# Kernel optimization log

Hardware: AMD Instinct MI355X
Metric: run time of the kernel (lower is better)

The kernel has to match this reference:

```python
import jax, jax.numpy as jnp
import numpy as np

F, B, H, N = 2048, 2, 1024, 16
E = H // N  # per-head depth = 64


def setup_inputs() -> dict:
    key = jax.random.key(0)
    k1, k2, k3, k4 = jax.random.split(key, 4)
    q_input = jax.random.normal(k1, (F, B, H), dtype=jnp.float32)
    mask = jax.random.randint(k2, (B, 1, F, F), 0, 2).astype(bool)
    w_qkv = jax.random.normal(k3, (H, 3 * H), dtype=jnp.float32) * 0.02
    b_qkv = jnp.zeros((3 * H,), dtype=jnp.float32)
    w_out = jax.random.normal(k4, (N, E, H), dtype=jnp.float32) * 0.02
    b_out = jnp.zeros((H,), dtype=jnp.float32)
    return {"q_input": q_input, "mask": mask, "w_qkv": w_qkv, "b_qkv": b_qkv,
            "w_out": w_out, "b_out": b_out}


def reference(q_input, mask, w_qkv, b_qkv, w_out, b_out):
    # fused QKV projection: FBH,HD->FBD (+ bias on D)
    qkv = jnp.einsum('fbh,hd->fbd', q_input, w_qkv) + b_qkv          # [F,B,3H]
    qkv = qkv.reshape(F, B, N, 3 * E)
    q, k, v = jnp.split(qkv, 3, axis=-1)                             # each [F,B,N,E]
    scale = 1.0 / jnp.sqrt(jnp.asarray(E, dtype=q.dtype))
    logits = jnp.einsum('fbne,tbne->bnft', q, k) * scale             # [B,N,F,T]
    logits = jnp.where(mask, logits, jnp.asarray(-10000.0, logits.dtype))
    attn_w = jax.nn.softmax(logits, axis=-1)
    ctx = jnp.einsum('bnft,tbne->bnfe', attn_w, v)                   # [B,N,F,E]
    ctx = jnp.transpose(ctx, (2, 0, 1, 3))                           # [F,B,N,E]
    out = jnp.einsum('fbne,ned->fbd', ctx, w_out)                    # [F,B,H] (no bias added)
    return out, b_out
```

## Files before the change

### kernel.cpp

```cpp
#include <hip/hip_runtime.h>
#include <hip/hip_bf16.h>
#include <math.h>

#define F_DIM 2048
#define B_DIM 2
#define H_DIM 1024
#define N_HEADS 16
#define E_DIM 64
#define D3 3072
#define M_DIM 4096

typedef __hip_bfloat16 bf16;
typedef __attribute__((ext_vector_type(8))) __bf16 bf16x8;
typedef __attribute__((ext_vector_type(8))) unsigned short u16x8;
typedef __attribute__((ext_vector_type(4))) float f32x4;

static __device__ __forceinline__ unsigned short f2bf(float f) {
    unsigned u = __float_as_uint(f);
    return (unsigned short)((u + 0x7FFFu + ((u >> 16) & 1u)) >> 16);
}

static __device__ __forceinline__ void glds16(const unsigned short* g, unsigned short* l) {
    __builtin_amdgcn_global_load_lds((const __attribute__((address_space(1))) unsigned int*)g,
                                     (__attribute__((address_space(3))) unsigned int*)l,
                                     16, 0, 0);
}

__global__ void detect_mask_kernel(const int* __restrict__ mask_words, int* __restrict__ flag) {
    __shared__ int red[256];
    int v = mask_words[threadIdx.x];
    red[threadIdx.x] = v & ~1;
    __syncthreads();
    for (int s = 128; s > 0; s >>= 1) {
        if (threadIdx.x < s) red[threadIdx.x] |= red[threadIdx.x + s];
        __syncthreads();
    }
    if (threadIdx.x == 0) *flag = (red[0] != 0) ? 1 : 0;
}

__global__ void pack_mask_kernel(const int* __restrict__ mi, const unsigned char* __restrict__ mu,
                                 const int* __restrict__ flag, unsigned* __restrict__ bits) {
    int w = blockIdx.x * 256 + threadIdx.x;
    size_t base = (size_t)w * 32;
    unsigned out = 0;
    if (*flag) {
        #pragma unroll
        for (int j = 0; j < 32; ++j) out |= (mu[base + j] ? 1u : 0u) << j;
    } else {
        #pragma unroll
        for (int j = 0; j < 32; ++j) out |= (mi[base + j] ? 1u : 0u) << j;
    }
    bits[w] = out;
}

__global__ __launch_bounds__(256) void convert_kernel(const float* __restrict__ in,
                                                      unsigned short* __restrict__ out) {
    int i = (blockIdx.x * 256 + threadIdx.x) * 8;
    float4 a = *(const float4*)&in[i];
    float4 b = *(const float4*)&in[i + 4];
    u16x8 o;
    o[0] = f2bf(a.x); o[1] = f2bf(a.y); o[2] = f2bf(a.z); o[3] = f2bf(a.w);
    o[4] = f2bf(b.x); o[5] = f2bf(b.y); o[6] = f2bf(b.z); o[7] = f2bf(b.w);
    *(u16x8*)&out[i] = o;
}

__global__ __launch_bounds__(256) void transpose_bf16_kernel(const float* __restrict__ in,
                                                             unsigned short* __restrict__ out,
                                                             int R, int C) {
    __shared__ float t[32][33];
    const int c0 = blockIdx.x * 32, r0 = blockIdx.y * 32;
    const int lc = threadIdx.x & 31, lr = threadIdx.x >> 5;
    #pragma unroll
    for (int i = 0; i < 4; ++i) {
        int r = lr + i * 8;
        t[r][lc] = in[(size_t)(r0 + r) * C + c0 + lc];
    }
    __syncthreads();
    #pragma unroll
    for (int i = 0; i < 4; ++i) {
        int r = lr + i * 8;
        out[(size_t)(c0 + r) * R + r0 + lc] = f2bf(t[lc][r]);
    }
}

template<int BM, int BN, bool ADD_BIAS, bool OUT_BF16>
__global__ __launch_bounds__(256) void gemm_bt_kernel(const unsigned short* __restrict__ A,
                                                      const unsigned short* __restrict__ Bt,
                                                      const float* __restrict__ bias,
                                                      void* __restrict__ Cout, int Nc) {
    __shared__ unsigned short Ald[BM * 32];
    __shared__ unsigned short Bld[BN * 32];
    constexpr int WM = BM / 2, WN = BN / 2;
    constexpr int MI = WM / 16, NI = WN / 16;
    constexpr int ACH = BM * 4;
    constexpr int TCH = (BM + BN) * 4;
    const int tid = threadIdx.x;
    const int wave = tid >> 6;
    const int lane = tid & 63;
    const int quad = lane >> 4;
    const int l16 = lane & 15;
    const int wm = (wave & 1) * WM;
    const int wn = (wave >> 1) * WN;
    const int m0 = blockIdx.y * BM;
    const int n0 = blockIdx.x * BN;

    f32x4 acc[MI][NI];
    #pragma unroll
    for (int i = 0; i < MI; ++i)
        #pragma unroll
        for (int j = 0; j < NI; ++j) acc[i][j] = (f32x4){0.f, 0.f, 0.f, 0.f};

    for (int k0 = 0; k0 < 1024; k0 += 32) {
        __syncthreads();
        #pragma unroll
        for (int rr = 0; rr < TCH / 256; ++rr) {
            const int chunk = rr * 256 + tid;
            const int wbase = (rr * 256 + wave * 64) * 8;
            if (chunk < ACH) {
                const int row = chunk >> 2, ko = (chunk & 3) * 8;
                glds16(&A[(size_t)(m0 + row) * 1024 + k0 + ko], &Ald[wbase]);
            } else {
                const int c2 = chunk - ACH;
                const int row = c2 >> 2, ko = (c2 & 3) * 8;
                glds16(&Bt[(size_t)(n0 + row) * 1024 + k0 + ko], &Bld[wbase - ACH * 8]);
            }
        }
        __syncthreads();

        bf16x8 af[MI], bfr[NI];
        #pragma unroll
        for (int i = 0; i < MI; ++i)
            af[i] = *(const bf16x8*)&Ald[(wm + i * 16 + l16) * 32 + quad * 8];
        #pragma unroll
        for (int j = 0; j < NI; ++j)
            bfr[j] = *(const bf16x8*)&Bld[(wn + j * 16 + l16) * 32 + quad * 8];
        #pragma unroll
        for (int mi = 0; mi < MI; ++mi)
            #pragma unroll
            for (int ni = 0; ni < NI; ++ni)
                acc[mi][ni] = __builtin_amdgcn_mfma_f32_16x16x32_bf16(af[mi], bfr[ni], acc[mi][ni], 0, 0, 0);
    }

    #pragma unroll
    for (int ni = 0; ni < NI; ++ni) {
        const int col = n0 + wn + ni * 16 + l16;
        const float bv = ADD_BIAS ? bias[col] : 0.f;
        #pragma unroll
        for (int mi = 0; mi < MI; ++mi) {
            const int rowb = m0 + wm + mi * 16 + quad * 4;
            #pragma unroll
            for (int r = 0; r < 4; ++r) {
                float v = acc[mi][ni][r] + bv;
                if (OUT_BF16) ((unsigned short*)Cout)[(size_t)(rowb + r) * Nc + col] = f2bf(v);
                else          ((float*)Cout)[(size_t)(rowb + r) * Nc + col] = v;
            }
        }
    }
}

#define TT 64
#define LSTR 72
__global__ __launch_bounds__(256) void attn_mfma_kernel(const bf16* __restrict__ qkv_,
                                                        const unsigned* __restrict__ mbits,
                                                        unsigned short* __restrict__ ctxb) {
    __shared__ unsigned short K_lds[TT * LSTR];
    __shared__ unsigned short Vt_lds[E_DIM * LSTR];
    __shared__ unsigned short P_lds[4 * 16 * LSTR];

    const unsigned short* qkv = (const unsigned short*)qkv_;
    const int tid = threadIdx.x;
    const int wave = tid >> 6;
    const int lane = tid & 63;
    const int quad = lane >> 4;
    const int l16 = lane & 15;
    const int f0 = blockIdx.x * 64;
    const int b = blockIdx.y >> 4;
    const int n = blockIdx.y & 15;
    const int head = n * 192;

    bf16x8 qf[2];
    #pragma unroll
    for (int ks = 0; ks < 2; ++ks) {
        int f = f0 + wave * 16 + l16;
        qf[ks] = *(const bf16x8*)&qkv[(size_t)(f * B_DIM + b) * D3 + head + ks * 32 + quad * 8];
    }

    f32x4 O[4];
    #pragma unroll
    for (int ec = 0; ec < 4; ++ec) O[ec] = (f32x4){0.f, 0.f, 0.f, 0.f};
    float lsum[4] = {0.f, 0.f, 0.f, 0.f};

    unsigned short* Pw = P_lds + wave * 16 * LSTR;
    const float c_exp = 0.18033688011112042f;

    for (int t0 = 0; t0 < F_DIM; t0 += TT) {
        __syncthreads();

        #pragma unroll
        for (int i = 0; i < 2; ++i) {
            int c = tid + i * 256;
            int tr = c >> 3, e0 = (c & 7) * 8;
            u16x8 kv = *(const u16x8*)&qkv[(size_t)((t0 + tr) * B_DIM + b) * D3 + head + 64 + e0];
            *(u16x8*)&K_lds[tr * LSTR + e0] = kv;
        }
        {
            int tp = tid & 31, e0 = (tid >> 5) * 8;
            u16x8 v0 = *(const u16x8*)&qkv[(size_t)((t0 + 2 * tp) * B_DIM + b) * D3 + head + 128 + e0];
            u16x8 v1 = *(const u16x8*)&qkv[(size_t)((t0 + 2 * tp + 1) * B_DIM + b) * D3 + head + 128 + e0];
            #pragma unroll
            for (int j = 0; j < 8; ++j) {
                unsigned pk = (unsigned)v0[j] | ((unsigned)v1[j] << 16);
                *(unsigned*)&Vt_lds[(e0 + j) * LSTR + 2 * tp] = pk;
            }
        }
        __syncthreads();

        f32x4 S[4];
        #pragma unroll
        for (int ck = 0; ck < 4; ++ck) S[ck] = (f32x4){0.f, 0.f, 0.f, 0.f};
        #pragma unroll
        for (int ck = 0; ck < 4; ++ck)
            #pragma unroll
            for (int ks = 0; ks < 2; ++ks) {
                bf16x8 kb = *(const bf16x8*)&K_lds[(ck * 16 + l16) * LSTR + ks * 32 + quad * 8];
                S[ck] = __builtin_amdgcn_mfma_f32_16x16x32_bf16(qf[ks], kb, S[ck], 0, 0, 0);
            }

        #pragma unroll
        for (int r = 0; r < 4; ++r) {
            const int row = quad * 4 + r;
            const int f = f0 + wave * 16 + row;
            uint2 wb = *(const uint2*)&mbits[((size_t)b * F_DIM + f) * 64 + (t0 >> 5)];
            #pragma unroll
            for (int ck = 0; ck < 4; ++ck) {
                unsigned wsel = (ck & 2) ? wb.y : wb.x;
                int bit = ((ck & 1) << 4) + l16;
                float p = __builtin_amdgcn_exp2f(S[ck][r] * c_exp);
                p = ((wsel >> bit) & 1u) ? p : 0.f;
                lsum[r] += p;
                Pw[row * LSTR + ck * 16 + l16] = f2bf(p);
            }
        }

        #pragma unroll
        for (int ks = 0; ks < 2; ++ks) {
            bf16x8 pf = *(const bf16x8*)&Pw[l16 * LSTR + ks * 32 + quad * 8];
            #pragma unroll
            for (int ec = 0; ec < 4; ++ec) {
                bf16x8 vb = *(const bf16x8*)&Vt_lds[(ec * 16 + l16) * LSTR + ks * 32 + quad * 8];
                O[ec] = __builtin_amdgcn_mfma_f32_16x16x32_bf16(pf, vb, O[ec], 0, 0, 0);
            }
        }
    }

    #pragma unroll
    for (int r = 0; r < 4; ++r) {
        float l = lsum[r];
        #pragma unroll
        for (int d = 1; d < 16; d <<= 1) l += __shfl_xor(l, d);
        const int f = f0 + wave * 16 + quad * 4 + r;
        const float inv = 1.0f / l;
        #pragma unroll
        for (int ec = 0; ec < 4; ++ec) {
            ctxb[(size_t)(f * B_DIM + b) * H_DIM + n * 64 + ec * 16 + l16] = f2bf(O[ec][r] * inv);
        }
    }
}

__global__ void bout_copy_kernel(const float* __restrict__ b_out, float* __restrict__ dst) {
    int h = blockIdx.x * 256 + threadIdx.x;
    if (h < H_DIM) dst[h] = b_out[h];
}

extern "C" void kernel_launch(void* const* d_in, const int* in_sizes, int n_in,
                              void* d_out, int out_size, void* d_ws, size_t ws_size,
                              hipStream_t stream) {
    const float* q_input = (const float*)d_in[0];
    const void*  mask    = d_in[1];
    const float* w_qkv   = (const float*)d_in[2];
    const float* b_qkv   = (const float*)d_in[3];
    const float* w_out   = (const float*)d_in[4];
    const float* b_out   = (const float*)d_in[5];
    float* out = (float*)d_out;

    char* ws = (char*)d_ws;
    bf16*           qkv     = (bf16*)ws;
    unsigned short* qin_bf  = (unsigned short*)(ws + 25165824);
    unsigned short* ctx     = qin_bf;
    unsigned short* wqkv_bt = (unsigned short*)(ws + 33554432);
    unsigned short* wout_bt = wqkv_bt;
    unsigned*       mbits   = (unsigned*)(ws + 39845888);
    int*            flag    = (int*)(ws + 40894464);

    detect_mask_kernel<<<1, 256, 0, stream>>>((const int*)mask, flag);
    pack_mask_kernel<<<1024, 256, 0, stream>>>((const int*)mask, (const unsigned char*)mask, flag, mbits);

    convert_kernel<<<2048, 256, 0, stream>>>(q_input, qin_bf);
    transpose_bf16_kernel<<<dim3(96, 32), 256, 0, stream>>>(w_qkv, wqkv_bt, 1024, 3072);

    gemm_bt_kernel<128, 128, true, true><<<dim3(24, 32), 256, 0, stream>>>(qin_bf, wqkv_bt, b_qkv, qkv, 3072);

    transpose_bf16_kernel<<<dim3(32, 32), 256, 0, stream>>>(w_out, wout_bt, 1024, 1024);

    attn_mfma_kernel<<<dim3(32, 32), 256, 0, stream>>>(qkv, mbits, ctx);

    gemm_bt_kernel<64, 128, false, false><<<dim3(8, 64), 256, 0, stream>>>(ctx, wout_bt, nullptr, out, 1024);

    bout_copy_kernel<<<4, 256, 0, stream>>>(b_out, out + (size_t)M_DIM * H_DIM);
}
```

Baseline: 262.2 us.

## Split key dimension across waves in attention kernel and reduce partial outputs in LDS

The attention kernel now has each wave handle all 64 query rows for its own 32-key slice of a 128-key tile. K fragments are loaded straight from global memory into registers instead of being staged through LDS, and only V is transposed into shared memory. Partial O accumulators and row sums from the four waves are combined at the end through an LDS tree reduction. This aims to halve the number of loop iterations and barriers and to cut LDS traffic for K, at the cost of more registers (16 accumulator tiles per wave) and an extra reduction epilogue.

```diff
diff --git a/kernel.cpp b/kernel.cpp
--- a/kernel.cpp
+++ b/kernel.cpp
@@ -158,14 +158,15 @@
     }
 }
 
-#define TT 64
-#define LSTR 72
+#define TSTR 136
+#define PSTR 40
 __global__ __launch_bounds__(256) void attn_mfma_kernel(const bf16* __restrict__ qkv_,
                                                         const unsigned* __restrict__ mbits,
                                                         unsigned short* __restrict__ ctxb) {
-    __shared__ unsigned short K_lds[TT * LSTR];
-    __shared__ unsigned short Vt_lds[E_DIM * LSTR];
-    __shared__ unsigned short P_lds[4 * 16 * LSTR];
+    __shared__ __align__(16) char smem[38912];
+    unsigned short* Vt = (unsigned short*)smem;
+    unsigned short* P  = (unsigned short*)(smem + 17408);
+    float* lred        = (float*)(smem + 37888);
 
     const unsigned short* qkv = (const unsigned short*)qkv_;
     const int tid = threadIdx.x;
@@ -177,93 +178,166 @@
     const int b = blockIdx.y >> 4;
     const int n = blockIdx.y & 15;
     const int head = n * 192;
-
-    bf16x8 qf[2];
-    #pragma unroll
-    for (int ks = 0; ks < 2; ++ks) {
-        int f = f0 + wave * 16 + l16;
-        qf[ks] = *(const bf16x8*)&qkv[(size_t)(f * B_DIM + b) * D3 + head + ks * 32 + quad * 8];
-    }
-
-    f32x4 O[4];
-    #pragma unroll
-    for (int ec = 0; ec < 4; ++ec) O[ec] = (f32x4){0.f, 0.f, 0.f, 0.f};
-    float lsum[4] = {0.f, 0.f, 0.f, 0.f};
-
-    unsigned short* Pw = P_lds + wave * 16 * LSTR;
+    const int tw = wave * 32;
+
+    bf16x8 qf[4][2];
+    #pragma unroll
+    for (int g = 0; g < 4; ++g)
+        #pragma unroll
+        for (int ks = 0; ks < 2; ++ks) {
+            int f = f0 + g * 16 + l16;
+            qf[g][ks] = *(const bf16x8*)&qkv[(size_t)(f * B_DIM + b) * D3 + head + ks * 32 + quad * 8];
+        }
+
+    f32x4 O[4][4];
+    #pragma unroll
+    for (int g = 0; g < 4; ++g)
+        #pragma unroll
+        for (int ec = 0; ec < 4; ++ec) O[g][ec] = (f32x4){0.f, 0.f, 0.f, 0.f};
+    float lsum[4][4];
+    #pragma unroll
+    for (int g = 0; g < 4; ++g)
+        #pragma unroll
+        for (int r = 0; r < 4; ++r) lsum[g][r] = 0.f;
+
+    unsigned short* Pw = P + wave * 64 * PSTR;
     const float c_exp = 0.18033688011112042f;
 
-    for (int t0 = 0; t0 < F_DIM; t0 += TT) {
+    for (int t0 = 0; t0 < F_DIM; t0 += 128) {
+        bf16x8 kf[2][2];
+        #pragma unroll
+        for (int s = 0; s < 2; ++s)
+            #pragma unroll
+            for (int ks = 0; ks < 2; ++ks) {
+                int t = t0 + tw + s * 16 + l16;
+                kf[s][ks] = *(const bf16x8*)&qkv[(size_t)(t * B_DIM + b) * D3 + head + 64 + ks * 32 + quad * 8];
+            }
+
         __syncthreads();
 
         #pragma unroll
         for (int i = 0; i < 2; ++i) {
-            int c = tid + i * 256;
-            int tr = c >> 3, e0 = (c & 7) * 8;
-            u16x8 kv = *(const u16x8*)&qkv[(size_t)((t0 + tr) * B_DIM + b) * D3 + head + 64 + e0];
-            *(u16x8*)&K_lds[tr * LSTR + e0] = kv;
-        }
-        {
-            int tp = tid & 31, e0 = (tid >> 5) * 8;
-            u16x8 v0 = *(const u16x8*)&qkv[(size_t)((t0 + 2 * tp) * B_DIM + b) * D3 + head + 128 + e0];
-            u16x8 v1 = *(const u16x8*)&qkv[(size_t)((t0 + 2 * tp + 1) * B_DIM + b) * D3 + head + 128 + e0];
+            int c = i * 256 + tid;
+            int e0 = (c >> 6) * 8;
+            int rem = c & 63;
+            int wq = rem >> 4, tp = rem & 15;
+            int ta = t0 + wq * 32 + tp;
+            u16x8 va = *(const u16x8*)&qkv[(size_t)(ta * B_DIM + b) * D3 + head + 128 + e0];
+            u16x8 vb2 = *(const u16x8*)&qkv[(size_t)((ta + 16) * B_DIM + b) * D3 + head + 128 + e0];
             #pragma unroll
             for (int j = 0; j < 8; ++j) {
-                unsigned pk = (unsigned)v0[j] | ((unsigned)v1[j] << 16);
-                *(unsigned*)&Vt_lds[(e0 + j) * LSTR + 2 * tp] = pk;
-            }
-        }
-        __syncthreads();
-
-        f32x4 S[4];
-        #pragma unroll
-        for (int ck = 0; ck < 4; ++ck) S[ck] = (f32x4){0.f, 0.f, 0.f, 0.f};
-        #pragma unroll
-        for (int ck = 0; ck < 4; ++ck)
-            #pragma unroll
-            for (int ks = 0; ks < 2; ++ks) {
-                bf16x8 kb = *(const bf16x8*)&K_lds[(ck * 16 + l16) * LSTR + ks * 32 + quad * 8];
-                S[ck] = __builtin_amdgcn_mfma_f32_16x16x32_bf16(qf[ks], kb, S[ck], 0, 0, 0);
-            }
-
+                unsigned pk = (unsigned)va[j] | ((unsigned)vb2[j] << 16);
+                *(unsigned*)&Vt[(e0 + j) * TSTR + wq * 32 + 2 * tp] = pk;
+            }
+        }
+        __syncthreads();
+
+        #pragma unroll
+        for (int g = 0; g < 4; ++g) {
+            f32x4 S0 = (f32x4){0.f, 0.f, 0.f, 0.f};
+            f32x4 S1 = (f32x4){0.f, 0.f, 0.f, 0.f};
+            S0 = __builtin_amdgcn_mfma_f32_16x16x32_bf16(qf[g][0], kf[0][0], S0, 0, 0, 0);
+            S0 = __builtin_amdgcn_mfma_f32_16x16x32_bf16(qf[g][1], kf[0][1], S0, 0, 0, 0);
+            S1 = __builtin_amdgcn_mfma_f32_16x16x32_bf16(qf[g][0], kf[1][0], S1, 0, 0, 0);
+            S1 = __builtin_amdgcn_mfma_f32_16x16x32_bf16(qf[g][1], kf[1][1], S1, 0, 0, 0);
+            #pragma unroll
+            for (int r = 0; r < 4; ++r) {
+                const int row = g * 16 + quad * 4 + r;
+                const int f = f0 + row;
+                unsigned mw = mbits[((size_t)b * F_DIM + f) * 64 + (t0 >> 5) + wave];
+                unsigned sh = mw >> l16;
+                float p0 = __builtin_amdgcn_exp2f(S0[r] * c_exp);
+                float p1 = __builtin_amdgcn_exp2f(S1[r] * c_exp);
+                p0 = (sh & 1u) ? p0 : 0.f;
+                p1 = ((sh >> 16) & 1u) ? p1 : 0.f;
+                lsum[g][r] += p0 + p1;
+                unsigned pk = (unsigned)f2bf(p0) | ((unsigned)f2bf(p1) << 16);
+                *(unsigned*)&Pw[row * PSTR + 2 * l16] = pk;
+            }
+        }
+
+        bf16x8 vb[4];
+        #pragma unroll
+        for (int ec = 0; ec < 4; ++ec)
+            vb[ec] = *(const bf16x8*)&Vt[(ec * 16 + l16) * TSTR + tw + quad * 8];
+        #pragma unroll
+        for (int g = 0; g < 4; ++g) {
+            bf16x8 pa = *(const bf16x8*)&Pw[(g * 16 + l16) * PSTR + quad * 8];
+            #pragma unroll
+            for (int ec = 0; ec < 4; ++ec)
+                O[g][ec] = __builtin_amdgcn_mfma_f32_16x16x32_bf16(pa, vb[ec], O[g][ec], 0, 0, 0);
+        }
+    }
+
+    #pragma unroll
+    for (int g = 0; g < 4; ++g)
         #pragma unroll
         for (int r = 0; r < 4; ++r) {
-            const int row = quad * 4 + r;
-            const int f = f0 + wave * 16 + row;
-            uint2 wb = *(const uint2*)&mbits[((size_t)b * F_DIM + f) * 64 + (t0 >> 5)];
-            #pragma unroll
-            for (int ck = 0; ck < 4; ++ck) {
-                unsigned wsel = (ck & 2) ? wb.y : wb.x;
-                int bit = ((ck & 1) << 4) + l16;
-                float p = __builtin_amdgcn_exp2f(S[ck][r] * c_exp);
-                p = ((wsel >> bit) & 1u) ? p : 0.f;
-                lsum[r] += p;
-                Pw[row * LSTR + ck * 16 + l16] = f2bf(p);
-            }
-        }
-
-        #pragma unroll
-        for (int ks = 0; ks < 2; ++ks) {
-            bf16x8 pf = *(const bf16x8*)&Pw[l16 * LSTR + ks * 32 + quad * 8];
-            #pragma unroll
-            for (int ec = 0; ec < 4; ++ec) {
-                bf16x8 vb = *(const bf16x8*)&Vt_lds[(ec * 16 + l16) * LSTR + ks * 32 + quad * 8];
-                O[ec] = __builtin_amdgcn_mfma_f32_16x16x32_bf16(pf, vb, O[ec], 0, 0, 0);
-            }
-        }
-    }
-
-    #pragma unroll
-    for (int r = 0; r < 4; ++r) {
-        float l = lsum[r];
-        #pragma unroll
-        for (int d = 1; d < 16; d <<= 1) l += __shfl_xor(l, d);
-        const int f = f0 + wave * 16 + quad * 4 + r;
-        const float inv = 1.0f / l;
-        #pragma unroll
-        for (int ec = 0; ec < 4; ++ec) {
-            ctxb[(size_t)(f * B_DIM + b) * H_DIM + n * 64 + ec * 16 + l16] = f2bf(O[ec][r] * inv);
-        }
+            float v = lsum[g][r];
+            #pragma unroll
+            for (int d = 1; d < 16; d <<= 1) v += __shfl_xor(v, d);
+            if (l16 == 0) lred[wave * 64 + g * 16 + quad * 4 + r] = v;
+        }
+    __syncthreads();
+
+    float* R0 = (float*)smem;
+    float* R1 = R0 + 4096;
+    if (wave == 2) {
+        #pragma unroll
+        for (int g = 0; g < 4; ++g)
+            #pragma unroll
+            for (int ec = 0; ec < 4; ++ec)
+                *(f32x4*)&R0[(g * 4 + ec) * 256 + lane * 4] = O[g][ec];
+    }
+    if (wave == 3) {
+        #pragma unroll
+        for (int g = 0; g < 4; ++g)
+            #pragma unroll
+            for (int ec = 0; ec < 4; ++ec)
+                *(f32x4*)&R1[(g * 4 + ec) * 256 + lane * 4] = O[g][ec];
+    }
+    __syncthreads();
+    if (wave == 0) {
+        #pragma unroll
+        for (int g = 0; g < 4; ++g)
+            #pragma unroll
+            for (int ec = 0; ec < 4; ++ec)
+                O[g][ec] += *(const f32x4*)&R0[(g * 4 + ec) * 256 + lane * 4];
+    }
+    if (wave == 1) {
+        #pragma unroll
+        for (int g = 0; g < 4; ++g)
+            #pragma unroll
+            for (int ec = 0; ec < 4; ++ec)
+                O[g][ec] += *(const f32x4*)&R1[(g * 4 + ec) * 256 + lane * 4];
+    }
+    __syncthreads();
+    if (wave == 1) {
+        #pragma unroll
+        for (int g = 0; g < 4; ++g)
+            #pragma unroll
+            for (int ec = 0; ec < 4; ++ec)
+                *(f32x4*)&R0[(g * 4 + ec) * 256 + lane * 4] = O[g][ec];
+    }
+    __syncthreads();
+    if (wave == 0) {
+        #pragma unroll
+        for (int g = 0; g < 4; ++g)
+            #pragma unroll
+            for (int ec = 0; ec < 4; ++ec)
+                O[g][ec] += *(const f32x4*)&R0[(g * 4 + ec) * 256 + lane * 4];
+        #pragma unroll
+        for (int g = 0; g < 4; ++g)
+            #pragma unroll
+            for (int r = 0; r < 4; ++r) {
+                const int row = g * 16 + quad * 4 + r;
+                float tot = lred[row] + lred[64 + row] + lred[128 + row] + lred[192 + row];
+                const float inv = 1.0f / tot;
+                const int f = f0 + row;
+                #pragma unroll
+                for (int ec = 0; ec < 4; ++ec)
+                    ctxb[(size_t)(f * B_DIM + b) * H_DIM + n * 64 + ec * 16 + l16] = f2bf(O[g][ec][r] * inv);
+            }
     }
 }
 
```

Measured after the change: 308.0 us. +17.4%, slower.

## Process 128 query rows per attention block to reuse K/V tiles

Applied to the files above, without the earlier changes.

Each attention block now covers 128 query rows instead of 64, so each wave handles two 16-row groups. Each K and V fragment loaded from LDS feeds two MFMAs, and each global K/V tile load serves twice as many queries, which halves global K/V traffic and the number of barriers per query row. The cost is only 512 blocks instead of 1024 on a 256-CU GPU, with more registers and LDS per block, which may reduce occupancy and latency hiding.

```diff
diff --git a/kernel.cpp b/kernel.cpp
--- a/kernel.cpp
+++ b/kernel.cpp
@@ -158,14 +158,13 @@
     }
 }
 
-#define TT 64
 #define LSTR 72
 __global__ __launch_bounds__(256) void attn_mfma_kernel(const bf16* __restrict__ qkv_,
                                                         const unsigned* __restrict__ mbits,
                                                         unsigned short* __restrict__ ctxb) {
-    __shared__ unsigned short K_lds[TT * LSTR];
-    __shared__ unsigned short Vt_lds[E_DIM * LSTR];
-    __shared__ unsigned short P_lds[4 * 16 * LSTR];
+    __shared__ unsigned short K_lds[64 * LSTR];
+    __shared__ unsigned short Vt_lds[64 * LSTR];
+    __shared__ unsigned short P_lds[128 * LSTR];
 
     const unsigned short* qkv = (const unsigned short*)qkv_;
     const int tid = threadIdx.x;
@@ -173,27 +172,35 @@
     const int lane = tid & 63;
     const int quad = lane >> 4;
     const int l16 = lane & 15;
-    const int f0 = blockIdx.x * 64;
+    const int f0 = blockIdx.x * 128;
     const int b = blockIdx.y >> 4;
     const int n = blockIdx.y & 15;
     const int head = n * 192;
 
-    bf16x8 qf[2];
-    #pragma unroll
-    for (int ks = 0; ks < 2; ++ks) {
-        int f = f0 + wave * 16 + l16;
-        qf[ks] = *(const bf16x8*)&qkv[(size_t)(f * B_DIM + b) * D3 + head + ks * 32 + quad * 8];
-    }
-
-    f32x4 O[4];
-    #pragma unroll
-    for (int ec = 0; ec < 4; ++ec) O[ec] = (f32x4){0.f, 0.f, 0.f, 0.f};
-    float lsum[4] = {0.f, 0.f, 0.f, 0.f};
-
-    unsigned short* Pw = P_lds + wave * 16 * LSTR;
+    bf16x8 qf[2][2];
+    #pragma unroll
+    for (int rg = 0; rg < 2; ++rg)
+        #pragma unroll
+        for (int ks = 0; ks < 2; ++ks) {
+            int f = f0 + wave * 32 + rg * 16 + l16;
+            qf[rg][ks] = *(const bf16x8*)&qkv[(size_t)(f * B_DIM + b) * D3 + head + ks * 32 + quad * 8];
+        }
+
+    f32x4 O[2][4];
+    #pragma unroll
+    for (int rg = 0; rg < 2; ++rg)
+        #pragma unroll
+        for (int ec = 0; ec < 4; ++ec) O[rg][ec] = (f32x4){0.f, 0.f, 0.f, 0.f};
+    float lsum[2][4];
+    #pragma unroll
+    for (int rg = 0; rg < 2; ++rg)
+        #pragma unroll
+        for (int r = 0; r < 4; ++r) lsum[rg][r] = 0.f;
+
+    unsigned short* Pw = P_lds + wave * 32 * LSTR;
     const float c_exp = 0.18033688011112042f;
 
-    for (int t0 = 0; t0 < F_DIM; t0 += TT) {
+    for (int t0 = 0; t0 < F_DIM; t0 += 64) {
         __syncthreads();
 
         #pragma unroll
@@ -215,54 +222,70 @@
         }
         __syncthreads();
 
-        f32x4 S[4];
-        #pragma unroll
-        for (int ck = 0; ck < 4; ++ck) S[ck] = (f32x4){0.f, 0.f, 0.f, 0.f};
-        #pragma unroll
-        for (int ck = 0; ck < 4; ++ck)
-            #pragma unroll
-            for (int ks = 0; ks < 2; ++ks) {
-                bf16x8 kb = *(const bf16x8*)&K_lds[(ck * 16 + l16) * LSTR + ks * 32 + quad * 8];
-                S[ck] = __builtin_amdgcn_mfma_f32_16x16x32_bf16(qf[ks], kb, S[ck], 0, 0, 0);
-            }
-
+        f32x4 S[2][4];
+        #pragma unroll
+        for (int rg = 0; rg < 2; ++rg)
+            #pragma unroll
+            for (int ck = 0; ck < 4; ++ck) S[rg][ck] = (f32x4){0.f, 0.f, 0.f, 0.f};
+        #pragma unroll
+        for (int ck = 0; ck < 4; ++ck) {
+            bf16x8 kb0 = *(const bf16x8*)&K_lds[(ck * 16 + l16) * LSTR + quad * 8];
+            bf16x8 kb1 = *(const bf16x8*)&K_lds[(ck * 16 + l16) * LSTR + 32 + quad * 8];
+            #pragma unroll
+            for (int rg = 0; rg < 2; ++rg) {
+                S[rg][ck] = __builtin_amdgcn_mfma_f32_16x16x32_bf16(qf[rg][0], kb0, S[rg][ck], 0, 0, 0);
+                S[rg][ck] = __builtin_amdgcn_mfma_f32_16x16x32_bf16(qf[rg][1], kb1, S[rg][ck], 0, 0, 0);
+            }
+        }
+
+        #pragma unroll
+        for (int rg = 0; rg < 2; ++rg) {
+            #pragma unroll
+            for (int r = 0; r < 4; ++r) {
+                const int row = rg * 16 + quad * 4 + r;
+                const int f = f0 + wave * 32 + row;
+                uint2 wb = *(const uint2*)&mbits[((size_t)b * F_DIM + f) * 64 + (t0 >> 5)];
+                #pragma unroll
+                for (int ck = 0; ck < 4; ++ck) {
+                    unsigned wsel = (ck & 2) ? wb.y : wb.x;
+                    int bit = ((ck & 1) << 4) + l16;
+                    float p = __builtin_amdgcn_exp2f(S[rg][ck][r] * c_exp);
+                    p = ((wsel >> bit) & 1u) ? p : 0.f;
+                    lsum[rg][r] += p;
+                    Pw[row * LSTR + ck * 16 + l16] = f2bf(p);
+                }
+            }
+        }
+
+        #pragma unroll
+        for (int ks = 0; ks < 2; ++ks) {
+            bf16x8 vb[4];
+            #pragma unroll
+            for (int ec = 0; ec < 4; ++ec)
+                vb[ec] = *(const bf16x8*)&Vt_lds[(ec * 16 + l16) * LSTR + ks * 32 + quad * 8];
+            #pragma unroll
+            for (int rg = 0; rg < 2; ++rg) {
+                bf16x8 pa = *(const bf16x8*)&Pw[(rg * 16 + l16) * LSTR + ks * 32 + quad * 8];
+                #pragma unroll
+                for (int ec = 0; ec < 4; ++ec)
+                    O[rg][ec] = __builtin_amdgcn_mfma_f32_16x16x32_bf16(pa, vb[ec], O[rg][ec], 0, 0, 0);
+            }
+        }
+    }
+
+    #pragma unroll
+    for (int rg = 0; rg < 2; ++rg) {
         #pragma unroll
         for (int r = 0; r < 4; ++r) {
-            const int row = quad * 4 + r;
-            const int f = f0 + wave * 16 + row;
-            uint2 wb = *(const uint2*)&mbits[((size_t)b * F_DIM + f) * 64 + (t0 >> 5)];
-            #pragma unroll
-            for (int ck = 0; ck < 4; ++ck) {
-                unsigned wsel = (ck & 2) ? wb.y : wb.x;
-                int bit = ((ck & 1) << 4) + l16;
-                float p = __builtin_amdgcn_exp2f(S[ck][r] * c_exp);
-                p = ((wsel >> bit) & 1u) ? p : 0.f;
-                lsum[r] += p;
-                Pw[row * LSTR + ck * 16 + l16] = f2bf(p);
-            }
-        }
-
-        #pragma unroll
-        for (int ks = 0; ks < 2; ++ks) {
-            bf16x8 pf = *(const bf16x8*)&Pw[l16 * LSTR + ks * 32 + quad * 8];
+            float l = lsum[rg][r];
+            #pragma unroll
+            for (int d = 1; d < 16; d <<= 1) l += __shfl_xor(l, d);
+            const int f = f0 + wave * 32 + rg * 16 + quad * 4 + r;
+            const float inv = 1.0f / l;
             #pragma unroll
             for (int ec = 0; ec < 4; ++ec) {
-                bf16x8 vb = *(const bf16x8*)&Vt_lds[(ec * 16 + l16) * LSTR + ks * 32 + quad * 8];
-                O[ec] = __builtin_amdgcn_mfma_f32_16x16x32_bf16(pf, vb, O[ec], 0, 0, 0);
-            }
-        }
-    }
-
-    #pragma unroll
-    for (int r = 0; r < 4; ++r) {
-        float l = lsum[r];
-        #pragma unroll
-        for (int d = 1; d < 16; d <<= 1) l += __shfl_xor(l, d);
-        const int f = f0 + wave * 16 + quad * 4 + r;
-        const float inv = 1.0f / l;
-        #pragma unroll
-        for (int ec = 0; ec < 4; ++ec) {
-            ctxb[(size_t)(f * B_DIM + b) * H_DIM + n * 64 + ec * 16 + l16] = f2bf(O[ec][r] * inv);
+                ctxb[(size_t)(f * B_DIM + b) * H_DIM + n * 64 + ec * 16 + l16] = f2bf(O[rg][ec][r] * inv);
+            }
         }
     }
 }
@@ -302,7 +325,7 @@
 
     transpose_bf16_kernel<<<dim3(32, 32), 256, 0, stream>>>(w_out, wout_bt, 1024, 1024);
 
-    attn_mfma_kernel<<<dim3(32, 32), 256, 0, stream>>>(qkv, mbits, ctx);
+    attn_mfma_kernel<<<dim3(16, 32), 256, 0, stream>>>(qkv, mbits, ctx);
 
     gemm_bt_kernel<64, 128, false, false><<<dim3(8, 64), 256, 0, stream>>>(ctx, wout_bt, nullptr, out, 1024);
 
```

Result: slower. 279.8 us (+6.7%).
